# Kernel tuning notes

Hardware: AMD Instinct MI355X
Metric: run time of the kernel (lower is better)

## Reference

```python
import jax, jax.numpy as jnp
import numpy as np

B, N, F = 4, 4096, 32
NG = 14  # number of gate graph-convs in GCNLSTM_Cell with memory state


def setup_inputs() -> dict:
    key = jax.random.key(0)
    ks = jax.random.split(key, 7)
    x = jax.random.normal(ks[0], (B, N, F), jnp.float32)
    h = jax.random.normal(ks[1], (B, N, F), jnp.float32)
    c = jax.random.normal(ks[2], (B, N, F), jnp.float32)
    m = jax.random.normal(ks[3], (B, N, F), jnp.float32)
    # weighted dense adjacency, scaled so row sums are O(1)
    adj = jax.random.uniform(ks[4], (N, N), jnp.float32) / N
    # 14 WeightedGraphConv layers: Dense F -> 2F (single FeedForward layer, no relu)
    W = jax.random.normal(ks[5], (NG, F, 2 * F), jnp.float32) * (1.0 / np.sqrt(F))
    b = jnp.zeros((NG, 2 * F), jnp.float32)
    return {"x": x, "h": h, "c": c, "m": m, "adj": adj, "W": W, "b": b}


def _gcn(ax, W, b):
    # ax: [B,N,F] = adj @ state (precomputed); Dense to 2F then GLU split.
    z = ax @ W + b  # [B,N,2F]
    ls, rs = jnp.split(z, 2, axis=-1)
    return ls * jax.nn.sigmoid(rs)


def reference(x, h, c, m, adj, W, b):
    # shared graph aggregation for x and h (adj is the same for all gates)
    ax = jnp.einsum('nm,bmf->bnf', adj, x)  # [B,N,F]
    ah = jnp.einsum('nm,bmf->bnf', adj, h)

    fx = _gcn(ax, W[0], b[0]); fh = _gcn(ah, W[1], b[1])
    ix = _gcn(ax, W[2], b[2]); ih = _gcn(ah, W[3], b[3])
    cx = _gcn(ax, W[4], b[4]); ch = _gcn(ah, W[5], b[5])
    ox = _gcn(ax, W[6], b[6]); oh = _gcn(ah, W[7], b[7])

    f = jax.nn.sigmoid(fx + fh)
    i = jax.nn.sigmoid(ix + ih)
    o = jax.nn.sigmoid(ox + oh)
    c_new = f * c + i * jnp.tanh(cx + ch)
    h1 = o * jnp.tanh(c_new)

    # memory-state block (6 more graph convs on h1 and m)
    ah1 = jnp.einsum('nm,bmf->bnf', adj, h1)
    am = jnp.einsum('nm,bmf->bnf', adj, m)
    sa_ih = _gcn(ah1, W[8], b[8]);  sa_im = _gcn(am, W[9], b[9])
    sa_gh = _gcn(ah1, W[10], b[10]); sa_gm = _gcn(am, W[11], b[11])
    sa_oh = _gcn(ah1, W[12], b[12]); sa_om = _gcn(am, W[13], b[13])

    i2 = jax.nn.sigmoid(sa_ih + sa_im)
    g = jax.nn.sigmoid(sa_gh + sa_gm)
    o2 = jax.nn.sigmoid(sa_oh + sa_om)
    m_new = i2 * m + (1.0 - i2) * g
    h_new = m_new * o2
    return h_new, c_new, m_new
```

## Files before the change

kernel.cpp:

```cpp
#include <hip/hip_runtime.h>
#include <stdint.h>

typedef __attribute__((ext_vector_type(4))) float f32x4;
typedef __attribute__((ext_vector_type(8))) short s16x8;

#define BB 4
#define NN 4096
#define FF 32
#define BNF (BB*NN*FF)

typedef __attribute__((address_space(3))) void       as3_void;
typedef const __attribute__((address_space(1))) void as1_cvoid;

static __device__ __forceinline__ float bf2f(uint16_t u) {
    union { uint32_t i; float f; } v; v.i = ((uint32_t)u) << 16; return v.f;
}
static __device__ __forceinline__ uint16_t f2bf(float f) {
    union { float f; uint32_t i; } v; v.f = f;
    uint32_t r = v.i + 0x7FFFu + ((v.i >> 16) & 1u);
    return (uint16_t)(r >> 16);
}
static __device__ __forceinline__ float sig_acc(float x) { return 1.0f / (1.0f + expf(-x)); }

__global__ __launch_bounds__(256) void prep_kernel(
    const float* __restrict__ adj, uint16_t* __restrict__ adjb, int cvtN,
    const float* __restrict__ Wf, uint16_t* __restrict__ Wp,
    const float* __restrict__ x, const float* __restrict__ h,
    const float* __restrict__ m,
    uint16_t* __restrict__ P, uint16_t* __restrict__ P2)
{
    int bid = blockIdx.x;
    int t = threadIdx.x;

    if (bid < cvtN) {
        size_t i = ((size_t)bid * 256 + t) * 8;
        float4 v0 = *(const float4*)(adj + i);
        float4 v1 = *(const float4*)(adj + i + 4);
        union { uint4 u; uint16_t e[8]; } o;
        o.e[0] = f2bf(v0.x); o.e[1] = f2bf(v0.y); o.e[2] = f2bf(v0.z); o.e[3] = f2bf(v0.w);
        o.e[4] = f2bf(v1.x); o.e[5] = f2bf(v1.y); o.e[6] = f2bf(v1.z); o.e[7] = f2bf(v1.w);
        *(uint4*)(adjb + i) = o.u;
        return;
    }
    bid -= cvtN;

    if (bid < 112) {
        int idx = bid * 256 + t;
        int g   = idx >> 11;
        int k   = (idx >> 6) & 31;
        int col = idx & 63;
        uint16_t v = f2bf(Wf[idx]);
        int gp = g >> 1;
        int sl = ((g & 1) << 2) | (k >> 3);
        int ph = sl ^ (col & 7);
        Wp[((gp * 64 + col) * 64) + ph * 8 + (k & 7)] = v;
        return;
    }
    bid -= 112;

    const float* src; uint16_t* dst; int rowbase, b, n0;
    if (bid < 512) {
        int tensor = bid >> 8;
        src = tensor ? h : x; dst = P; rowbase = tensor * 128;
        b = (bid >> 6) & 3; n0 = (bid & 63) * 64;
    } else {
        int q = bid - 512;
        src = m; dst = P2; rowbase = 128;
        b = q >> 6; n0 = (q & 63) * 64;
    }
    __shared__ uint16_t tl[32][65];
    {
        int i = t >> 2, ch = t & 3;
        size_t idx = ((size_t)(b * NN + n0 + i)) * FF + ch * 8;
        float4 v0 = *(const float4*)(src + idx);
        float4 v1 = *(const float4*)(src + idx + 4);
        uint16_t e[8] = { f2bf(v0.x), f2bf(v0.y), f2bf(v0.z), f2bf(v0.w),
                          f2bf(v1.x), f2bf(v1.y), f2bf(v1.z), f2bf(v1.w) };
        #pragma unroll
        for (int k = 0; k < 8; k++) tl[ch * 8 + k][i] = e[k];
    }
    __syncthreads();
    {
        int f = t >> 3, ch = t & 7;
        union { uint4 u; uint16_t e[8]; } v;
        #pragma unroll
        for (int k = 0; k < 8; k++) v.e[k] = tl[f][ch * 8 + k];
        size_t row = (size_t)(rowbase + b * 32 + f);
        *(uint4*)(dst + row * NN + n0 + ch * 8) = v.u;
    }
}

__global__ __launch_bounds__(256) void gemm_kernel(
    const void* __restrict__ Av,
    const uint16_t* __restrict__ Bt,
    uint16_t* __restrict__ Cb,
    int isf32A)
{
    int nt = blockIdx.x, mt = blockIdx.y;
    int m0 = mt * 16, c0 = nt * 64;
    __shared__ __align__(16) uint16_t aL[4][16 * 32];
    __shared__ __align__(16) uint16_t bL[4][64 * 32];
    int t = threadIdx.x;
    int lane = t & 63, w = t >> 6;
    int lm = lane & 15, lk = lane >> 4;

    const uint16_t* A16 = (const uint16_t*)Av;
    const float*    Af  = (const float*)Av;

    f32x4 acc = {};

    for (int kk = 0; kk < 4096; kk += 128) {
        if (!isf32A) {
            {
                int q = t >> 6, pos = (t & 63) * 16;
                int row = pos >> 6;
                int slot = ((pos >> 4) & 3) ^ ((row >> 1) & 3);
                size_t aidx = (size_t)(m0 + row) * 4096 + kk + q * 32 + slot * 8;
                __builtin_amdgcn_global_load_lds((as1_cvoid*)(A16 + aidx),
                    (as3_void*)((char*)aL[q] + pos), 16, 0, 0);
            }
            #pragma unroll
            for (int q = 0; q < 4; q++) {
                int pos = t * 16;
                int row = pos >> 6;
                int slot = ((pos >> 4) & 3) ^ ((row >> 1) & 3);
                size_t bidx = (size_t)(c0 + row) * 4096 + kk + q * 32 + slot * 8;
                __builtin_amdgcn_global_load_lds((as1_cvoid*)(Bt + bidx),
                    (as3_void*)((char*)bL[q] + pos), 16, 0, 0);
            }
        } else {
            union { uint4 u; uint16_t e[8]; } sa, sb[4];
            int aq = t >> 6, apos = (t & 63) * 16;
            {
                int row = apos >> 6;
                int slot = ((apos >> 4) & 3) ^ ((row >> 1) & 3);
                size_t aidx = (size_t)(m0 + row) * 4096 + kk + aq * 32 + slot * 8;
                union { uint4 u[2]; float f[8]; } va;
                va.u[0] = *(const uint4*)(Af + aidx);
                va.u[1] = *(const uint4*)(Af + aidx + 4);
                #pragma unroll
                for (int k = 0; k < 8; k++) sa.e[k] = f2bf(va.f[k]);
            }
            #pragma unroll
            for (int q = 0; q < 4; q++) {
                int pos = t * 16;
                int row = pos >> 6;
                int slot = ((pos >> 4) & 3) ^ ((row >> 1) & 3);
                size_t bidx = (size_t)(c0 + row) * 4096 + kk + q * 32 + slot * 8;
                sb[q].u = *(const uint4*)(Bt + bidx);
            }
            *(uint4*)((char*)aL[aq] + apos) = sa.u;
            #pragma unroll
            for (int q = 0; q < 4; q++)
                *(uint4*)((char*)bL[q] + t * 16) = sb[q].u;
        }
        __syncthreads();
        {
            int rA = lm,          swA = (lk ^ ((rA >> 1) & 3)) * 8;
            int rB = w * 16 + lm, swB = (lk ^ ((rB >> 1) & 3)) * 8;
            #pragma unroll
            for (int q = 0; q < 4; q++) {
                s16x8 af = *(const s16x8*)(aL[q] + rA * 32 + swA);
                s16x8 bf = *(const s16x8*)(bL[q] + rB * 32 + swB);
                acc = __builtin_amdgcn_mfma_f32_16x16x32_bf16(af, bf, acc, 0, 0, 0);
            }
        }
        __syncthreads();
    }

    {
        int c = c0 + w * 16 + lm;
        int mr = m0 + lk * 4;
        union { uint2 u; uint16_t e[4]; } v;
        #pragma unroll
        for (int r = 0; r < 4; r++) v.e[r] = f2bf(acc[r]);
        *(uint2*)(Cb + (size_t)c * 4096 + mr) = v.u;
    }
}

__global__ __launch_bounds__(256) void fuse1_kernel(
    const uint16_t* __restrict__ Cbi,
    const uint16_t* __restrict__ Wp,
    const float* __restrict__ bf_,
    const float* __restrict__ cf,
    float* __restrict__ cnew, uint16_t* __restrict__ S2t)
{
    __shared__ float    AL[64 * 17];
    __shared__ float    SX[4][64][9];
    __shared__ uint16_t H1[32 * 18];

    int t = threadIdx.x;
    int bid = blockIdx.x;
    int b = bid >> 8, n0 = (bid & 255) * 16;
    int lane = t & 63, w = t >> 6;
    int j = lane & 15, kg = lane >> 4;
    int ej = t & 15, erow = (t >> 4) & 15;

    float cv[2];
    #pragma unroll
    for (int hh = 0; hh < 2; hh++)
        cv[hh] = cf[((size_t)(b * NN + n0 + erow)) * FF + ej + hh * 16];

    {
        int r = t >> 2, ch = t & 3;
        int crow = (r < 32) ? (b * 32 + r) : (128 + b * 32 + (r - 32));
        const uint16_t* cp = Cbi + (size_t)crow * 4096 + n0 + ch * 4;
        uint2 v = *(const uint2*)cp;
        const uint16_t* pe = (const uint16_t*)&v;
        #pragma unroll
        for (int e = 0; e < 4; e++) AL[r * 17 + ch * 4 + e] = bf2f(pe[e]);
    }
    __syncthreads();

    s16x8 a_ax, a_ah;
    #pragma unroll
    for (int e = 0; e < 8; e++) {
        int k = kg * 8 + e;
        a_ax[e] = (short)f2bf(AL[k * 17 + j]);
        a_ah[e] = (short)f2bf(AL[(32 + k) * 17 + j]);
    }
    {
        int p = w;
        int g0 = p * 2, g1 = p * 2 + 1;
        f32x4 ac0[4] = {}, ac1[4] = {};
        #pragma unroll
        for (int ct = 0; ct < 4; ct++) {
            int col = ct * 16 + j;
            int ph0 = (kg)     ^ (col & 7);
            int ph1 = (4 + kg) ^ (col & 7);
            s16x8 b0 = *(const s16x8*)(Wp + (p * 64 + col) * 64 + ph0 * 8);
            s16x8 b1 = *(const s16x8*)(Wp + (p * 64 + col) * 64 + ph1 * 8);
            ac0[ct] = __builtin_amdgcn_mfma_f32_16x16x32_bf16(a_ax, b0, ac0[ct], 0, 0, 0);
            ac1[ct] = __builtin_amdgcn_mfma_f32_16x16x32_bf16(a_ah, b1, ac1[ct], 0, 0, 0);
        }
        #pragma unroll
        for (int hh = 0; hh < 2; hh++)
            #pragma unroll
            for (int r = 0; r < 4; r++) {
                float z0l = ac0[hh][r]     + bf_[g0 * 64 + hh * 16 + j];
                float z0r = ac0[2 + hh][r] + bf_[g0 * 64 + 32 + hh * 16 + j];
                float z1l = ac1[hh][r]     + bf_[g1 * 64 + hh * 16 + j];
                float z1r = ac1[2 + hh][r] + bf_[g1 * 64 + 32 + hh * 16 + j];
                SX[p][lane][hh * 4 + r] = z0l * sig_acc(z0r) + z1l * sig_acc(z1r);
            }
    }
    __syncthreads();

    {
        int pl = ((erow >> 2) << 4) | ej;
        int ridx = erow & 3;
        #pragma unroll
        for (int hh = 0; hh < 2; hh++) {
            float s0 = SX[0][pl][hh * 4 + ridx];
            float s1 = SX[1][pl][hh * 4 + ridx];
            float s2 = SX[2][pl][hh * 4 + ridx];
            float s3 = SX[3][pl][hh * 4 + ridx];
            float fg = sig_acc(s0), ig = sig_acc(s1);
            float cc = tanhf(s2),   og = sig_acc(s3);
            float cn = fg * cv[hh] + ig * cc;
            size_t gidx = ((size_t)(b * NN + n0 + erow)) * FF + ej + hh * 16;
            cnew[gidx] = cn;
            H1[(ej + hh * 16) * 18 + erow] = f2bf(og * tanhf(cn));
        }
    }
    __syncthreads();
    if (t < 64) {
        int f = t >> 1, half = t & 1;
        union { uint4 u; uint16_t e[8]; } v;
        #pragma unroll
        for (int k = 0; k < 8; k++) v.e[k] = H1[f * 18 + half * 8 + k];
        *(uint4*)(S2t + ((size_t)(b * 32 + f)) * NN + n0 + half * 8) = v.u;
    }
}

__global__ __launch_bounds__(256) void fuse2_kernel(
    const uint16_t* __restrict__ Cbi,
    const uint16_t* __restrict__ Wp,
    const float* __restrict__ bf_,
    const float* __restrict__ mf,
    float* __restrict__ hnew, float* __restrict__ mnew)
{
    __shared__ float AL[64 * 17];
    __shared__ float SX[3][64][9];

    int t = threadIdx.x;
    int bid = blockIdx.x;
    int b = bid >> 8, n0 = (bid & 255) * 16;
    int lane = t & 63, w = t >> 6;
    int j = lane & 15, kg = lane >> 4;
    int ej = t & 15, erow = (t >> 4) & 15;

    float mv[2];
    #pragma unroll
    for (int hh = 0; hh < 2; hh++)
        mv[hh] = mf[((size_t)(b * NN + n0 + erow)) * FF + ej + hh * 16];

    {
        int r = t >> 2, ch = t & 3;
        int crow = (r < 32) ? (b * 32 + r) : (128 + b * 32 + (r - 32));
        const uint16_t* cp = Cbi + (size_t)crow * 4096 + n0 + ch * 4;
        uint2 v = *(const uint2*)cp;
        const uint16_t* pe = (const uint16_t*)&v;
        #pragma unroll
        for (int e = 0; e < 4; e++) AL[r * 17 + ch * 4 + e] = bf2f(pe[e]);
    }
    __syncthreads();

    if (w < 3) {
        s16x8 a_h1, a_m;
        #pragma unroll
        for (int e = 0; e < 8; e++) {
            int k = kg * 8 + e;
            a_h1[e] = (short)f2bf(AL[k * 17 + j]);
            a_m[e]  = (short)f2bf(AL[(32 + k) * 17 + j]);
        }
        const uint16_t* WpG = Wp + 4 * 64 * 64;
        const float*    bG  = bf_ + 512;
        int p = w;
        int g0 = p * 2, g1 = p * 2 + 1;
        f32x4 ac0[4] = {}, ac1[4] = {};
        #pragma unroll
        for (int ct = 0; ct < 4; ct++) {
            int col = ct * 16 + j;
            int ph0 = (kg)     ^ (col & 7);
            int ph1 = (4 + kg) ^ (col & 7);
            s16x8 b0 = *(const s16x8*)(WpG + (p * 64 + col) * 64 + ph0 * 8);
            s16x8 b1 = *(const s16x8*)(WpG + (p * 64 + col) * 64 + ph1 * 8);
            ac0[ct] = __builtin_amdgcn_mfma_f32_16x16x32_bf16(a_h1, b0, ac0[ct], 0, 0, 0);
            ac1[ct] = __builtin_amdgcn_mfma_f32_16x16x32_bf16(a_m, b1, ac1[ct], 0, 0, 0);
        }
        #pragma unroll
        for (int hh = 0; hh < 2; hh++)
            #pragma unroll
            for (int r = 0; r < 4; r++) {
                float z0l = ac0[hh][r]     + bG[g0 * 64 + hh * 16 + j];
                float z0r = ac0[2 + hh][r] + bG[g0 * 64 + 32 + hh * 16 + j];
                float z1l = ac1[hh][r]     + bG[g1 * 64 + hh * 16 + j];
                float z1r = ac1[2 + hh][r] + bG[g1 * 64 + 32 + hh * 16 + j];
                SX[p][lane][hh * 4 + r] = z0l * sig_acc(z0r) + z1l * sig_acc(z1r);
            }
    }
    __syncthreads();

    {
        int pl = ((erow >> 2) << 4) | ej;
        int ridx = erow & 3;
        #pragma unroll
        for (int hh = 0; hh < 2; hh++) {
            float s0 = SX[0][pl][hh * 4 + ridx];
            float s1 = SX[1][pl][hh * 4 + ridx];
            float s2 = SX[2][pl][hh * 4 + ridx];
            float i2 = sig_acc(s0);
            float gg = sig_acc(s1);
            float o2 = sig_acc(s2);
            float mn = i2 * mv[hh] + (1.0f - i2) * gg;
            size_t gidx = ((size_t)(b * NN + n0 + erow)) * FF + ej + hh * 16;
            mnew[gidx] = mn;
            hnew[gidx] = mn * o2;
        }
    }
}

extern "C" void kernel_launch(void* const* d_in, const int* in_sizes, int n_in,
                              void* d_out, int out_size, void* d_ws, size_t ws_size,
                              hipStream_t stream) {
    (void)in_sizes; (void)n_in; (void)out_size;
    const float* x   = (const float*)d_in[0];
    const float* h   = (const float*)d_in[1];
    const float* c   = (const float*)d_in[2];
    const float* m   = (const float*)d_in[3];
    const float* adj = (const float*)d_in[4];
    const float* W   = (const float*)d_in[5];
    const float* bb  = (const float*)d_in[6];
    float* out = (float*)d_out;

    char* ws = (char*)d_ws;
    int haveAdjb = ws_size >= (size_t)(40u << 20);
    uint16_t* adjb = (uint16_t*)ws;
    size_t pOff = haveAdjb ? (size_t)(32u << 20) : 0;
    uint16_t* P    = (uint16_t*)(ws + pOff);
    uint16_t* P2   = (uint16_t*)(ws + pOff + (2u << 20));
    uint16_t* Cbuf = (uint16_t*)(ws + pOff + (4u << 20));
    uint16_t* Wp   = (uint16_t*)(ws + pOff + (6u << 20));

    if (ws_size < (8u << 20)) return;

    const void* Agemm = haveAdjb ? (const void*)adjb : (const void*)adj;
    int isf32A = haveAdjb ? 0 : 1;
    int cvtN = haveAdjb ? 8192 : 0;

    prep_kernel<<<cvtN + 112 + 768, 256, 0, stream>>>(adj, adjb, cvtN, W, Wp, x, h, m, P, P2);

    gemm_kernel<<<dim3(4, 256), 256, 0, stream>>>(Agemm, P, Cbuf, isf32A);
    fuse1_kernel<<<1024, 256, 0, stream>>>(Cbuf, Wp, bb, c, out + BNF, P2);
    gemm_kernel<<<dim3(4, 256), 256, 0, stream>>>(Agemm, P2, Cbuf, isf32A);
    fuse2_kernel<<<1024, 256, 0, stream>>>(Cbuf, Wp, bb, m, out, out + 2 * BNF);
}
```

Before: 198.9 us.

## Fuse adjacency GEMM into gate kernels and drop adj bf16 precast

Removes the standalone GEMM kernels and the prep pass that converted the full adjacency matrix to bf16. Each gate kernel now computes its own 16-row by 64-column adjacency product, converting fp32 adj tiles to bf16 on the fly, and keeps the accumulator in shared memory. This eliminates the intermediate Cbuf write and read, two kernel launches, and the 32 MB bf16 adj write. The cost is that each of the four batch blocks re-reads the fp32 adj tiles, which doubles the raw adj bytes per GEMM unless the cache absorbs the reuse. An occupancy hint of 3 blocks per CU is added.

```diff
diff --git a/kernel.cpp b/kernel.cpp
--- a/kernel.cpp
+++ b/kernel.cpp
@@ -23,7 +23,6 @@
 static __device__ __forceinline__ float sig_acc(float x) { return 1.0f / (1.0f + expf(-x)); }
 
 __global__ __launch_bounds__(256) void prep_kernel(
-    const float* __restrict__ adj, uint16_t* __restrict__ adjb, int cvtN,
     const float* __restrict__ Wf, uint16_t* __restrict__ Wp,
     const float* __restrict__ x, const float* __restrict__ h,
     const float* __restrict__ m,
@@ -31,18 +30,6 @@
 {
     int bid = blockIdx.x;
     int t = threadIdx.x;
-
-    if (bid < cvtN) {
-        size_t i = ((size_t)bid * 256 + t) * 8;
-        float4 v0 = *(const float4*)(adj + i);
-        float4 v1 = *(const float4*)(adj + i + 4);
-        union { uint4 u; uint16_t e[8]; } o;
-        o.e[0] = f2bf(v0.x); o.e[1] = f2bf(v0.y); o.e[2] = f2bf(v0.z); o.e[3] = f2bf(v0.w);
-        o.e[4] = f2bf(v1.x); o.e[5] = f2bf(v1.y); o.e[6] = f2bf(v1.z); o.e[7] = f2bf(v1.w);
-        *(uint4*)(adjb + i) = o.u;
-        return;
-    }
-    bid -= cvtN;
 
     if (bid < 112) {
         int idx = bid * 256 + t;
@@ -90,101 +77,16 @@
     }
 }
 
-__global__ __launch_bounds__(256) void gemm_kernel(
-    const void* __restrict__ Av,
-    const uint16_t* __restrict__ Bt,
-    uint16_t* __restrict__ Cb,
-    int isf32A)
-{
-    int nt = blockIdx.x, mt = blockIdx.y;
-    int m0 = mt * 16, c0 = nt * 64;
-    __shared__ __align__(16) uint16_t aL[4][16 * 32];
-    __shared__ __align__(16) uint16_t bL[4][64 * 32];
-    int t = threadIdx.x;
-    int lane = t & 63, w = t >> 6;
-    int lm = lane & 15, lk = lane >> 4;
-
-    const uint16_t* A16 = (const uint16_t*)Av;
-    const float*    Af  = (const float*)Av;
-
-    f32x4 acc = {};
-
-    for (int kk = 0; kk < 4096; kk += 128) {
-        if (!isf32A) {
-            {
-                int q = t >> 6, pos = (t & 63) * 16;
-                int row = pos >> 6;
-                int slot = ((pos >> 4) & 3) ^ ((row >> 1) & 3);
-                size_t aidx = (size_t)(m0 + row) * 4096 + kk + q * 32 + slot * 8;
-                __builtin_amdgcn_global_load_lds((as1_cvoid*)(A16 + aidx),
-                    (as3_void*)((char*)aL[q] + pos), 16, 0, 0);
-            }
-            #pragma unroll
-            for (int q = 0; q < 4; q++) {
-                int pos = t * 16;
-                int row = pos >> 6;
-                int slot = ((pos >> 4) & 3) ^ ((row >> 1) & 3);
-                size_t bidx = (size_t)(c0 + row) * 4096 + kk + q * 32 + slot * 8;
-                __builtin_amdgcn_global_load_lds((as1_cvoid*)(Bt + bidx),
-                    (as3_void*)((char*)bL[q] + pos), 16, 0, 0);
-            }
-        } else {
-            union { uint4 u; uint16_t e[8]; } sa, sb[4];
-            int aq = t >> 6, apos = (t & 63) * 16;
-            {
-                int row = apos >> 6;
-                int slot = ((apos >> 4) & 3) ^ ((row >> 1) & 3);
-                size_t aidx = (size_t)(m0 + row) * 4096 + kk + aq * 32 + slot * 8;
-                union { uint4 u[2]; float f[8]; } va;
-                va.u[0] = *(const uint4*)(Af + aidx);
-                va.u[1] = *(const uint4*)(Af + aidx + 4);
-                #pragma unroll
-                for (int k = 0; k < 8; k++) sa.e[k] = f2bf(va.f[k]);
-            }
-            #pragma unroll
-            for (int q = 0; q < 4; q++) {
-                int pos = t * 16;
-                int row = pos >> 6;
-                int slot = ((pos >> 4) & 3) ^ ((row >> 1) & 3);
-                size_t bidx = (size_t)(c0 + row) * 4096 + kk + q * 32 + slot * 8;
-                sb[q].u = *(const uint4*)(Bt + bidx);
-            }
-            *(uint4*)((char*)aL[aq] + apos) = sa.u;
-            #pragma unroll
-            for (int q = 0; q < 4; q++)
-                *(uint4*)((char*)bL[q] + t * 16) = sb[q].u;
-        }
-        __syncthreads();
-        {
-            int rA = lm,          swA = (lk ^ ((rA >> 1) & 3)) * 8;
-            int rB = w * 16 + lm, swB = (lk ^ ((rB >> 1) & 3)) * 8;
-            #pragma unroll
-            for (int q = 0; q < 4; q++) {
-                s16x8 af = *(const s16x8*)(aL[q] + rA * 32 + swA);
-                s16x8 bf = *(const s16x8*)(bL[q] + rB * 32 + swB);
-                acc = __builtin_amdgcn_mfma_f32_16x16x32_bf16(af, bf, acc, 0, 0, 0);
-            }
-        }
-        __syncthreads();
-    }
-
-    {
-        int c = c0 + w * 16 + lm;
-        int mr = m0 + lk * 4;
-        union { uint2 u; uint16_t e[4]; } v;
-        #pragma unroll
-        for (int r = 0; r < 4; r++) v.e[r] = f2bf(acc[r]);
-        *(uint2*)(Cb + (size_t)c * 4096 + mr) = v.u;
-    }
-}
-
-__global__ __launch_bounds__(256) void fuse1_kernel(
-    const uint16_t* __restrict__ Cbi,
+__global__ __launch_bounds__(256, 3) void mega1_kernel(
+    const float* __restrict__ adj,
+    const uint16_t* __restrict__ P,
     const uint16_t* __restrict__ Wp,
     const float* __restrict__ bf_,
     const float* __restrict__ cf,
     float* __restrict__ cnew, uint16_t* __restrict__ S2t)
 {
+    __shared__ __align__(16) uint16_t aLb[4][16 * 32];
+    __shared__ __align__(16) uint16_t bLb[4][64 * 32];
     __shared__ float    AL[64 * 17];
     __shared__ float    SX[4][64][9];
     __shared__ uint16_t H1[32 * 18];
@@ -193,7 +95,8 @@
     int bid = blockIdx.x;
     int b = bid >> 8, n0 = (bid & 255) * 16;
     int lane = t & 63, w = t >> 6;
-    int j = lane & 15, kg = lane >> 4;
+    int lm = lane & 15, lk = lane >> 4;
+    int j = lm, kg = lk;
     int ej = t & 15, erow = (t >> 4) & 15;
 
     float cv[2];
@@ -201,14 +104,49 @@
     for (int hh = 0; hh < 2; hh++)
         cv[hh] = cf[((size_t)(b * NN + n0 + erow)) * FF + ej + hh * 16];
 
-    {
-        int r = t >> 2, ch = t & 3;
-        int crow = (r < 32) ? (b * 32 + r) : (128 + b * 32 + (r - 32));
-        const uint16_t* cp = Cbi + (size_t)crow * 4096 + n0 + ch * 4;
-        uint2 v = *(const uint2*)cp;
-        const uint16_t* pe = (const uint16_t*)&v;
-        #pragma unroll
-        for (int e = 0; e < 4; e++) AL[r * 17 + ch * 4 + e] = bf2f(pe[e]);
+    int aq = t >> 6, apos = (t & 63) * 16;
+    int arow = apos >> 6;
+    int aslot = ((apos >> 4) & 3) ^ ((arow >> 1) & 3);
+    int bpos = t * 16;
+    int brow = bpos >> 6;
+    int bslot = ((bpos >> 4) & 3) ^ ((brow >> 1) & 3);
+    int bcrow = brow + ((brow < 32) ? b * 32 : 96 + b * 32);
+    int rA = lm;          int swA = (lk ^ ((rA >> 1) & 3)) * 8;
+    int rB = w * 16 + lm; int swB = (lk ^ ((rB >> 1) & 3)) * 8;
+
+    f32x4 acc = {};
+    for (int kk = 0; kk < 4096; kk += 128) {
+        {
+            size_t aidx = (size_t)(n0 + arow) * 4096 + kk + aq * 32 + aslot * 8;
+            union { uint4 u[2]; float f[8]; } va;
+            va.u[0] = *(const uint4*)(adj + aidx);
+            va.u[1] = *(const uint4*)(adj + aidx + 4);
+            union { uint4 u; uint16_t e[8]; } sa;
+            #pragma unroll
+            for (int k = 0; k < 8; k++) sa.e[k] = f2bf(va.f[k]);
+            *(uint4*)((char*)aLb[aq] + apos) = sa.u;
+        }
+        #pragma unroll
+        for (int q = 0; q < 4; q++) {
+            size_t bidx = (size_t)bcrow * 4096 + kk + q * 32 + bslot * 8;
+            __builtin_amdgcn_global_load_lds((as1_cvoid*)(P + bidx),
+                (as3_void*)((char*)bLb[q] + bpos), 16, 0, 0);
+        }
+        __syncthreads();
+        #pragma unroll
+        for (int q = 0; q < 4; q++) {
+            s16x8 af = *(const s16x8*)(aLb[q] + rA * 32 + swA);
+            s16x8 bf = *(const s16x8*)(bLb[q] + rB * 32 + swB);
+            acc = __builtin_amdgcn_mfma_f32_16x16x32_bf16(af, bf, acc, 0, 0, 0);
+        }
+        __syncthreads();
+    }
+
+    {
+        int cp = w * 16 + lm;
+        #pragma unroll
+        for (int r = 0; r < 4; r++)
+            AL[cp * 17 + lk * 4 + r] = acc[r];
     }
     __syncthreads();
 
@@ -273,13 +211,16 @@
     }
 }
 
-__global__ __launch_bounds__(256) void fuse2_kernel(
-    const uint16_t* __restrict__ Cbi,
+__global__ __launch_bounds__(256, 3) void mega2_kernel(
+    const float* __restrict__ adj,
+    const uint16_t* __restrict__ P2,
     const uint16_t* __restrict__ Wp,
     const float* __restrict__ bf_,
     const float* __restrict__ mf,
     float* __restrict__ hnew, float* __restrict__ mnew)
 {
+    __shared__ __align__(16) uint16_t aLb[4][16 * 32];
+    __shared__ __align__(16) uint16_t bLb[4][64 * 32];
     __shared__ float AL[64 * 17];
     __shared__ float SX[3][64][9];
 
@@ -287,7 +228,8 @@
     int bid = blockIdx.x;
     int b = bid >> 8, n0 = (bid & 255) * 16;
     int lane = t & 63, w = t >> 6;
-    int j = lane & 15, kg = lane >> 4;
+    int lm = lane & 15, lk = lane >> 4;
+    int j = lm, kg = lk;
     int ej = t & 15, erow = (t >> 4) & 15;
 
     float mv[2];
@@ -295,14 +237,49 @@
     for (int hh = 0; hh < 2; hh++)
         mv[hh] = mf[((size_t)(b * NN + n0 + erow)) * FF + ej + hh * 16];
 
-    {
-        int r = t >> 2, ch = t & 3;
-        int crow = (r < 32) ? (b * 32 + r) : (128 + b * 32 + (r - 32));
-        const uint16_t* cp = Cbi + (size_t)crow * 4096 + n0 + ch * 4;
-        uint2 v = *(const uint2*)cp;
-        const uint16_t* pe = (const uint16_t*)&v;
-        #pragma unroll
-        for (int e = 0; e < 4; e++) AL[r * 17 + ch * 4 + e] = bf2f(pe[e]);
+    int aq = t >> 6, apos = (t & 63) * 16;
+    int arow = apos >> 6;
+    int aslot = ((apos >> 4) & 3) ^ ((arow >> 1) & 3);
+    int bpos = t * 16;
+    int brow = bpos >> 6;
+    int bslot = ((bpos >> 4) & 3) ^ ((brow >> 1) & 3);
+    int bcrow = brow + ((brow < 32) ? b * 32 : 96 + b * 32);
+    int rA = lm;          int swA = (lk ^ ((rA >> 1) & 3)) * 8;
+    int rB = w * 16 + lm; int swB = (lk ^ ((rB >> 1) & 3)) * 8;
+
+    f32x4 acc = {};
+    for (int kk = 0; kk < 4096; kk += 128) {
+        {
+            size_t aidx = (size_t)(n0 + arow) * 4096 + kk + aq * 32 + aslot * 8;
+            union { uint4 u[2]; float f[8]; } va;
+            va.u[0] = *(const uint4*)(adj + aidx);
+            va.u[1] = *(const uint4*)(adj + aidx + 4);
+            union { uint4 u; uint16_t e[8]; } sa;
+            #pragma unroll
+            for (int k = 0; k < 8; k++) sa.e[k] = f2bf(va.f[k]);
+            *(uint4*)((char*)aLb[aq] + apos) = sa.u;
+        }
+        #pragma unroll
+        for (int q = 0; q < 4; q++) {
+            size_t bidx = (size_t)bcrow * 4096 + kk + q * 32 + bslot * 8;
+            __builtin_amdgcn_global_load_lds((as1_cvoid*)(P2 + bidx),
+                (as3_void*)((char*)bLb[q] + bpos), 16, 0, 0);
+        }
+        __syncthreads();
+        #pragma unroll
+        for (int q = 0; q < 4; q++) {
+            s16x8 af = *(const s16x8*)(aLb[q] + rA * 32 + swA);
+            s16x8 bf = *(const s16x8*)(bLb[q] + rB * 32 + swB);
+            acc = __builtin_amdgcn_mfma_f32_16x16x32_bf16(af, bf, acc, 0, 0, 0);
+        }
+        __syncthreads();
+    }
+
+    {
+        int cp = w * 16 + lm;
+        #pragma unroll
+        for (int r = 0; r < 4; r++)
+            AL[cp * 17 + lk * 4 + r] = acc[r];
     }
     __syncthreads();
 
@@ -375,24 +352,14 @@
     float* out = (float*)d_out;
 
     char* ws = (char*)d_ws;
-    int haveAdjb = ws_size >= (size_t)(40u << 20);
-    uint16_t* adjb = (uint16_t*)ws;
-    size_t pOff = haveAdjb ? (size_t)(32u << 20) : 0;
-    uint16_t* P    = (uint16_t*)(ws + pOff);
-    uint16_t* P2   = (uint16_t*)(ws + pOff + (2u << 20));
-    uint16_t* Cbuf = (uint16_t*)(ws + pOff + (4u << 20));
-    uint16_t* Wp   = (uint16_t*)(ws + pOff + (6u << 20));
-
-    if (ws_size < (8u << 20)) return;
-
-    const void* Agemm = haveAdjb ? (const void*)adjb : (const void*)adj;
-    int isf32A = haveAdjb ? 0 : 1;
-    int cvtN = haveAdjb ? 8192 : 0;
-
-    prep_kernel<<<cvtN + 112 + 768, 256, 0, stream>>>(adj, adjb, cvtN, W, Wp, x, h, m, P, P2);
-
-    gemm_kernel<<<dim3(4, 256), 256, 0, stream>>>(Agemm, P, Cbuf, isf32A);
-    fuse1_kernel<<<1024, 256, 0, stream>>>(Cbuf, Wp, bb, c, out + BNF, P2);
-    gemm_kernel<<<dim3(4, 256), 256, 0, stream>>>(Agemm, P2, Cbuf, isf32A);
-    fuse2_kernel<<<1024, 256, 0, stream>>>(Cbuf, Wp, bb, m, out, out + 2 * BNF);
-}
+    uint16_t* P    = (uint16_t*)ws;
+    uint16_t* P2   = (uint16_t*)(ws + (2u << 20));
+    uint16_t* Wp   = (uint16_t*)(ws + (4u << 20));
+
+    if (ws_size < (6u << 20)) return;
+
+    prep_kernel<<<880, 256, 0, stream>>>(W, Wp, x, h, m, P, P2);
+
+    mega1_kernel<<<1024, 256, 0, stream>>>(adj, P, Wp, bb, c, out + BNF, P2);
+    mega2_kernel<<<1024, 256, 0, stream>>>(adj, P2, Wp, bb, m, out, out + 2 * BNF);
+}
```

After: 187.3 us. 5.9% less time.
